# Optimization experiments

Measured on AMD Instinct MI355X. Metric: run time of the kernel, lower is better.

The kernel has to match this reference:

```python
import jax, jax.numpy as jnp
import numpy as np

B, T, C = 8, 2048, 1024   # batch, seq_len, n_embd
H = 128                   # head_size

def setup_inputs() -> dict:
    key = jax.random.key(0)
    kx, kk, kq, kv = jax.random.split(key, 4)
    scale = 1.0 / np.sqrt(C)
    return {
        "x": jax.random.normal(kx, (B, T, C), dtype=jnp.float32),
        "Wk": jax.random.normal(kk, (C, H), dtype=jnp.float32) * scale,
        "Wq": jax.random.normal(kq, (C, H), dtype=jnp.float32) * scale,
        "Wv": jax.random.normal(kv, (C, H), dtype=jnp.float32) * scale,
    }

def reference(x, Wk, Wq, Wv):
    # k,q,v: [B,T,H]
    k = x @ Wk
    q = x @ Wq
    v = x @ Wv
    # NOTE: original scales by C**-0.5 (n_embd), not head_size**-0.5
    wei = jnp.einsum("bth,bsh->bts", q, k) * (x.shape[-1] ** -0.5)  # [B,T,T]
    wei = jax.nn.softmax(wei, axis=-1)  # no causal mask in the source module
    # dropout = 0.0 -> identity
    out = jnp.einsum("bts,bsh->bth", wei, v)  # [B,T,H]
    return out
```

## Files before the change

kernel.cpp:

```cpp
#include <hip/hip_runtime.h>
#include <hip/hip_bf16.h>
#include <stdint.h>
#include <stddef.h>

#define NB 8
#define NT 2048
#define NC 1024
#define NH 128

typedef float f32x4 __attribute__((ext_vector_type(4)));
typedef short bf16x8 __attribute__((ext_vector_type(8)));
typedef short bf16x4 __attribute__((ext_vector_type(4)));

__device__ __forceinline__ unsigned short f2bf(float f) {
    union { float f; uint32_t u; } v; v.f = f;
    uint32_t u = v.u;
    u += 0x7fffu + ((u >> 16) & 1u);
    return (unsigned short)(u >> 16);
}

__device__ __forceinline__ void gld16(const void* gp, void* lp) {
    __builtin_amdgcn_global_load_lds(
        (const __attribute__((address_space(1))) unsigned int*)gp,
        (__attribute__((address_space(3))) unsigned int*)lp, 16, 0, 0);
}

__device__ __forceinline__ f32x4 mfma16(bf16x4 a, bf16x4 b, f32x4 c) {
#if __has_builtin(__builtin_amdgcn_mfma_f32_16x16x16_bf16)
    return __builtin_amdgcn_mfma_f32_16x16x16_bf16(a, b, c, 0, 0, 0);
#elif __has_builtin(__builtin_amdgcn_mfma_f32_16x16x16bf16_1k)
    return __builtin_amdgcn_mfma_f32_16x16x16bf16_1k(a, b, c, 0, 0, 0);
#else
    f32x4 d;
    asm volatile("v_mfma_f32_16x16x16_bf16 %0, %1, %2, %3"
                 : "=v"(d) : "v"(a), "v"(b), "v"(c));
    return d;
#endif
}


__global__ __launch_bounds__(256) void cast_w_kernel(const float* __restrict__ Wq,
                                                     const float* __restrict__ Wk,
                                                     const float* __restrict__ Wv,
                                                     unsigned short* __restrict__ Wtf) {
    int gid  = blockIdx.x * 256 + threadIdx.x;
    int lane = gid & 63;
    int fs   = gid >> 6;
    int kb   = fs & 31;
    int g    = fs >> 5;
    int w    = g >> 3;
    int g16  = g & 7;
    int quad = lane >> 4;
    int l16  = lane & 15;
    const float* src = (w == 0) ? Wq : ((w == 1) ? Wk : Wv);
    int n = g16 * 16 + l16;
    bf16x8 o;
#pragma unroll
    for (int j = 0; j < 8; ++j)
        o[j] = (short)f2bf(src[(size_t)(kb * 32 + quad * 8 + j) * 128 + n]);
    *(bf16x8*)(Wtf + (size_t)gid * 8) = o;
}

#define CS2 392

__global__ __launch_bounds__(512, 2) void proj_kernel(const float* __restrict__ x,
                                                      const unsigned short* __restrict__ Wtf,
                                                      unsigned short* __restrict__ Qf,
                                                      unsigned short* __restrict__ Kf,
                                                      unsigned short* __restrict__ Vf) {
    __shared__ __align__(16) unsigned short wbuf[4][24 * 512];
    __shared__ __align__(16) unsigned short abuf[2][64 * 128];

    const int tid  = threadIdx.x;
    const int wave = tid >> 6;
    const int lane = tid & 63;
    const int quad = lane >> 4;
    const int l16  = lane & 15;
    const int bidx = blockIdx.x;
    const int rowbase = bidx * 64;
    const int b    = bidx >> 5;
    const int mh   = wave & 1;
    const int nq   = wave >> 1;

    const int arow = wave * 8 + (lane >> 3);
    const float* axp = x + (size_t)(rowbase + arow) * NC;
    const int aswz = (arow & 7) << 3;
    const int rswz = (l16 & 7) << 3;

    float4 aS[2][4];
    f32x4 acc0[6] = {};
    f32x4 acc1[6] = {};

#define STAGE(KB, BI) { _Pragma("unroll") \
    for (int i_ = 0; i_ < 3; ++i_) { \
        const int g_ = wave * 3 + i_; \
        gld16(Wtf + ((size_t)(g_ * 32 + (KB)) * 512) + lane * 8, &wbuf[BI][g_ * 512]); } }

#define LOADA(C, S) { _Pragma("unroll") \
    for (int i_ = 0; i_ < 4; ++i_) \
        aS[S][i_] = *(const float4*)(axp + (C) * 128 + i_ * 32 + (lane & 7) * 4); }

#define DSWRITE(C, S) { _Pragma("unroll") \
    for (int i_ = 0; i_ < 4; ++i_) { \
        bf16x4 t_; \
        t_[0] = (short)f2bf(aS[S][i_].x); t_[1] = (short)f2bf(aS[S][i_].y); \
        t_[2] = (short)f2bf(aS[S][i_].z); t_[3] = (short)f2bf(aS[S][i_].w); \
        *(bf16x4*)(&abuf[(C) & 1][arow * 128 + ((i_ * 32 + (lane & 7) * 4) ^ aswz)]) = t_; } }

#define BARW(N) { asm volatile("s_waitcnt vmcnt(" #N ") lgkmcnt(0)" ::: "memory"); \
                  __builtin_amdgcn_s_barrier(); }

#define TICK(K, CUR) { \
    const unsigned short* ab_ = abuf[((K) >> 2) & 1]; \
    const int t2_ = ((K) & 3) * 32 + quad * 8; \
    bf16x8 af0 = *(const bf16x8*)(ab_ + (mh * 32 + l16) * 128 + (t2_ ^ rswz)); \
    bf16x8 af1 = *(const bf16x8*)(ab_ + (mh * 32 + 16 + l16) * 128 + (t2_ ^ rswz)); \
    _Pragma("unroll") \
    for (int i_ = 0; i_ < 6; ++i_) { \
        bf16x8 wf_ = *(const bf16x8*)(&wbuf[CUR][(nq * 6 + i_) * 512 + lane * 8]); \
        acc0[i_] = __builtin_amdgcn_mfma_f32_16x16x32_bf16(af0, wf_, acc0[i_], 0, 0, 0); \
        acc1[i_] = __builtin_amdgcn_mfma_f32_16x16x32_bf16(af1, wf_, acc1[i_], 0, 0, 0); } }

    LOADA(0, 0); LOADA(1, 1);
    STAGE(0, 0); STAGE(1, 1); STAGE(2, 2);
    asm volatile("s_waitcnt vmcnt(13)" ::: "memory");
    DSWRITE(0, 0);
    BARW(6);

    for (int c = 0; c < 6; ++c) {
        const int k0 = c * 4;
        LOADA(c + 2, c & 1);
        STAGE(k0 + 3, 3); TICK(k0 + 0, 0); BARW(10);
        STAGE(k0 + 4, 0); TICK(k0 + 1, 1); BARW(10);
        STAGE(k0 + 5, 1); TICK(k0 + 2, 2); BARW(6);
        STAGE(k0 + 6, 2); TICK(k0 + 3, 3); DSWRITE(c + 1, (c + 1) & 1); BARW(6);
    }
    STAGE(27, 3); TICK(24, 0); BARW(6);
    STAGE(28, 0); TICK(25, 1); BARW(6);
    STAGE(29, 1); TICK(26, 2); BARW(6);
    STAGE(30, 2); TICK(27, 3); DSWRITE(7, 1); BARW(6);
    STAGE(31, 3); TICK(28, 0); BARW(6);
    TICK(29, 1); BARW(3);
    TICK(30, 2); BARW(0);
    TICK(31, 3);
    asm volatile("s_waitcnt vmcnt(0) lgkmcnt(0)" ::: "memory");
    __builtin_amdgcn_s_barrier();

    unsigned short* cs = (unsigned short*)wbuf;
#pragma unroll
    for (int i = 0; i < 6; ++i) {
#pragma unroll
        for (int r = 0; r < 4; ++r) {
            cs[(mh * 32 +  0 + quad * 4 + r) * CS2 + nq * 96 + i * 16 + l16] = f2bf(acc0[i][r]);
            cs[(mh * 32 + 16 + quad * 4 + r) * CS2 + nq * 96 + i * 16 + l16] = f2bf(acc1[i][r]);
        }
    }
    __syncthreads();

    const int ibase = (rowbase & (NT - 1)) >> 4;
    unsigned short* qdst = Qf + (size_t)b * (NT * NH);
    unsigned short* kdst = Kf + (size_t)b * (NT * NH);
    unsigned short* vdst = Vf + (size_t)b * (NT * NH);

#pragma unroll
    for (int j = 0; j < 6; ++j) {
        const int s = wave * 6 + j;
        if (s < 32) {
            const int isK = s >> 4;
            const int t   = s & 15;
            const int m   = t >> 2;
            const int ks  = t & 3;
            unsigned short* dst = isK ? kdst : qdst;
            bf16x8 v = *(const bf16x8*)(&cs[(m * 16 + l16) * CS2 + isK * 128 + ks * 32 + quad * 8]);
            *(bf16x8*)(dst + ((size_t)((ibase + m) * 4 + ks) * 64 + lane) * 8) = v;
        } else {
            const int vv = s - 32;
            const int nt = vv >> 1;
            const int pp = vv & 1;
#pragma unroll
            for (int ff = 0; ff < 2; ++ff) {
                const int t4 = pp * 2 + ff;
                bf16x4 v;
#pragma unroll
                for (int jj = 0; jj < 4; ++jj)
                    v[jj] = (short)cs[(t4 * 16 + quad * 4 + jj) * CS2 + 256 + nt * 16 + l16];
                *(bf16x4*)(vdst + (size_t)(nt * 128 + ibase + t4) * 256 + lane * 4) = v;
            }
        }
    }

#undef TICK
#undef BARW
#undef DSWRITE
#undef LOADA
#undef STAGE
}

#define AKBUF(BI) (smem + (size_t)(BI) * 16384)
#define AVBUF(BI) (smem + (size_t)(BI) * 16384 + 8192)

__global__ __launch_bounds__(512, 1) void attn_kernel(const unsigned short* __restrict__ Qf,
                                                      const unsigned short* __restrict__ Kf,
                                                      const unsigned short* __restrict__ Vf,
                                                      float* __restrict__ out) {
    __shared__ __align__(16) unsigned short smem[3 * 16384];
    __shared__ float sl[8][32];

    const int tid  = threadIdx.x;
    const int wave = tid >> 6;
    const int lane = tid & 63;
    const int quad = lane >> 4;
    const int l16  = lane & 15;
    const int bid  = blockIdx.x;
    const int b    = bid & 7;
    const int iqg  = bid >> 3;
    const int mh   = wave & 1;
    const int kq   = wave >> 1;

    const unsigned short* qfp = Qf + (size_t)b * (NT * NH);
    const unsigned short* kfp = Kf + (size_t)b * (NT * NH);
    const unsigned short* vfp = Vf + (size_t)b * (NT * NH);

    const int iq0 = iqg * 4 + mh * 2;
    bf16x8 qf0[4], qf1[4];
#pragma unroll
    for (int ks = 0; ks < 4; ++ks) {
        qf0[ks] = *(const bf16x8*)(qfp + ((size_t)((iq0 + 0) * 4 + ks) * 64 + lane) * 8);
        qf1[ks] = *(const bf16x8*)(qfp + ((size_t)((iq0 + 1) * 4 + ks) * 64 + lane) * 8);
    }

    auto stage = [&](int j, int bi) {
#pragma unroll
        for (int i = 0; i < 4; ++i) {
            if (wave < 4) {
                const int fid = wave * 4 + i;
                gld16(kfp + ((size_t)(j * 16 + fid) * 512) + lane * 8, AKBUF(bi) + fid * 512);
            } else {
                const int sid = (wave - 4) * 4 + i;
                const int nt = sid >> 1;
                const int pp = sid & 1;
                gld16(vfp + ((size_t)(nt * 128 + j * 4 + pp * 2) * 256) + lane * 8,
                      AVBUF(bi) + (nt * 4 + pp * 2) * 256);
            }
        }
    };

    stage(0, 0);
    stage(1, 1);
    asm volatile("s_waitcnt vmcnt(4)" ::: "memory");
    __builtin_amdgcn_s_barrier();

    f32x4 O0[8] = {}, O1[8] = {};
    float ls0 = 0.f, ls1 = 0.f;
    const float scl2 = 0.03125f * 1.44269504088896340736f;

    int cur = 0;
    for (int j = 0; j < 32; ++j) {
        const int stb = (cur >= 1) ? cur - 1 : 2;
        if (j < 30) stage(j + 2, stb);
        const unsigned short* kb = AKBUF(cur);
        const unsigned short* vb = AVBUF(cur);

        f32x4 S0 = {}, S1 = {};
#pragma unroll
        for (int ks = 0; ks < 4; ++ks) {
            bf16x8 kf = *(const bf16x8*)(kb + (kq * 4 + ks) * 512 + lane * 8);
            S0 = __builtin_amdgcn_mfma_f32_16x16x32_bf16(kf, qf0[ks], S0, 0, 0, 0);
            S1 = __builtin_amdgcn_mfma_f32_16x16x32_bf16(kf, qf1[ks], S1, 0, 0, 0);
        }

        bf16x4 pf0, pf1;
#pragma unroll
        for (int r = 0; r < 4; ++r) {
            float p0 = __builtin_amdgcn_exp2f(S0[r] * scl2);
            float p1 = __builtin_amdgcn_exp2f(S1[r] * scl2);
            ls0 += p0;
            ls1 += p1;
            pf0[r] = (short)f2bf(p0);
            pf1[r] = (short)f2bf(p1);
        }

#pragma unroll
        for (int nt = 0; nt < 8; ++nt) {
            bf16x4 vf = *(const bf16x4*)(vb + (nt * 4 + kq) * 256 + lane * 4);
            O0[nt] = mfma16(pf0, vf, O0[nt]);
            O1[nt] = mfma16(pf1, vf, O1[nt]);
        }

        if (j < 30) {
            asm volatile("s_waitcnt vmcnt(4) lgkmcnt(0)" ::: "memory");
        } else {
            asm volatile("s_waitcnt vmcnt(0) lgkmcnt(0)" ::: "memory");
        }
        __builtin_amdgcn_s_barrier();
        cur = (cur >= 2) ? 0 : cur + 1;
    }

    ls0 += __shfl_xor(ls0, 16, 64);
    ls0 += __shfl_xor(ls0, 32, 64);
    ls1 += __shfl_xor(ls1, 16, 64);
    ls1 += __shfl_xor(ls1, 32, 64);
    if (quad == 0) {
        sl[wave][l16]      = ls0;
        sl[wave][16 + l16] = ls1;
    }

    float* od = (float*)smem;
    if (kq >= 2) {
        float* myod = od + (size_t)((kq - 2) * 2 + mh) * 32 * 132;
#pragma unroll
        for (int nt = 0; nt < 8; ++nt) {
#pragma unroll
            for (int r = 0; r < 4; ++r) {
                myod[(quad * 4 + r) * 132 + nt * 16 + l16]      = O0[nt][r];
                myod[(16 + quad * 4 + r) * 132 + nt * 16 + l16] = O1[nt][r];
            }
        }
    }
    __syncthreads();
    if (kq < 2) {
        const float* pod = od + (size_t)(kq * 2 + mh) * 32 * 132;
#pragma unroll
        for (int nt = 0; nt < 8; ++nt) {
#pragma unroll
            for (int r = 0; r < 4; ++r) {
                O0[nt][r] += pod[(quad * 4 + r) * 132 + nt * 16 + l16];
                O1[nt][r] += pod[(16 + quad * 4 + r) * 132 + nt * 16 + l16];
            }
        }
    }
    __syncthreads();
    if (kq == 1) {
        float* myod = od + (size_t)mh * 32 * 132;
#pragma unroll
        for (int nt = 0; nt < 8; ++nt) {
#pragma unroll
            for (int r = 0; r < 4; ++r) {
                myod[(quad * 4 + r) * 132 + nt * 16 + l16]      = O0[nt][r];
                myod[(16 + quad * 4 + r) * 132 + nt * 16 + l16] = O1[nt][r];
            }
        }
    }
    __syncthreads();

    if (kq == 0) {
        float inv0[4], inv1[4];
#pragma unroll
        for (int r = 0; r < 4; ++r) {
            const int rr = quad * 4 + r;
            inv0[r] = 1.0f / (sl[mh][rr] + sl[2 + mh][rr] +
                              sl[4 + mh][rr] + sl[6 + mh][rr]);
            inv1[r] = 1.0f / (sl[mh][16 + rr] + sl[2 + mh][16 + rr] +
                              sl[4 + mh][16 + rr] + sl[6 + mh][16 + rr]);
        }
        const float* pod = od + (size_t)mh * 32 * 132;
        float* orow = out + ((size_t)b * NT + iqg * 64 + mh * 32) * NH;
#pragma unroll
        for (int nt = 0; nt < 8; ++nt) {
#pragma unroll
            for (int r = 0; r < 4; ++r) {
                float v0 = O0[nt][r] + pod[(quad * 4 + r) * 132 + nt * 16 + l16];
                float v1 = O1[nt][r] + pod[(16 + quad * 4 + r) * 132 + nt * 16 + l16];
                orow[(quad * 4 + r) * NH + nt * 16 + l16]      = v0 * inv0[r];
                orow[(16 + quad * 4 + r) * NH + nt * 16 + l16] = v1 * inv1[r];
            }
        }
    }
}

#undef AKBUF
#undef AVBUF

extern "C" void kernel_launch(void* const* d_in, const int* in_sizes, int n_in,
                              void* d_out, int out_size, void* d_ws, size_t ws_size,
                              hipStream_t stream) {
    const float* x  = (const float*)d_in[0];
    const float* Wk = (const float*)d_in[1];
    const float* Wq = (const float*)d_in[2];
    const float* Wv = (const float*)d_in[3];
    float* out = (float*)d_out;

    char* ws = (char*)d_ws;
    unsigned short* Qf  = (unsigned short*)(ws);
    unsigned short* Kf  = (unsigned short*)(ws + 4194304);
    unsigned short* Vf  = (unsigned short*)(ws + 8388608);
    unsigned short* Wtf = (unsigned short*)(ws + 12582912);

    cast_w_kernel<<<192, 256, 0, stream>>>(Wq, Wk, Wv, Wtf);
    proj_kernel<<<256, 512, 0, stream>>>(x, Wtf, Qf, Kf, Vf);
    attn_kernel<<<256, 512, 0, stream>>>(Qf, Kf, Vf, out);
}
```

Measured before the change: 149.7 us.

## Restructure projection kernel to 32-row tiles with register-resident weight fragments

The projection kernel now uses 512 blocks of 256 threads, each computing 32 rows, instead of 256 blocks of 512 threads computing 64 rows. Weight fragments are loaded straight from global memory into registers, double-buffered two k-steps ahead, rather than staged through LDS with async global-to-LDS loads and many barriers. This cuts LDS use and barrier count and doubles the block count for better CU coverage. In exchange, each wave reads its weight slice from global/L2 with no cross-wave sharing, and global weight traffic doubles because each block covers fewer rows.

```diff
diff --git a/kernel.cpp b/kernel.cpp
--- a/kernel.cpp
+++ b/kernel.cpp
@@ -63,13 +63,12 @@
 
 #define CS2 392
 
-__global__ __launch_bounds__(512, 2) void proj_kernel(const float* __restrict__ x,
-                                                      const unsigned short* __restrict__ Wtf,
-                                                      unsigned short* __restrict__ Qf,
-                                                      unsigned short* __restrict__ Kf,
-                                                      unsigned short* __restrict__ Vf) {
-    __shared__ __align__(16) unsigned short wbuf[4][24 * 512];
-    __shared__ __align__(16) unsigned short abuf[2][64 * 128];
+__global__ __launch_bounds__(256) void proj_kernel(const float* __restrict__ x,
+                                                   const unsigned short* __restrict__ Wtf,
+                                                   unsigned short* __restrict__ Qf,
+                                                   unsigned short* __restrict__ Kf,
+                                                   unsigned short* __restrict__ Vf) {
+    __shared__ __align__(16) unsigned short smem[12800];
 
     const int tid  = threadIdx.x;
     const int wave = tid >> 6;
@@ -77,82 +76,73 @@
     const int quad = lane >> 4;
     const int l16  = lane & 15;
     const int bidx = blockIdx.x;
-    const int rowbase = bidx * 64;
-    const int b    = bidx >> 5;
-    const int mh   = wave & 1;
-    const int nq   = wave >> 1;
-
-    const int arow = wave * 8 + (lane >> 3);
+    const int rowbase = bidx * 32;
+    const int b    = bidx >> 6;
+
+    const int arow = tid >> 3;
     const float* axp = x + (size_t)(rowbase + arow) * NC;
     const int aswz = (arow & 7) << 3;
     const int rswz = (l16 & 7) << 3;
 
     float4 aS[2][4];
+    bf16x8 wA[6], wB[6];
     f32x4 acc0[6] = {};
     f32x4 acc1[6] = {};
 
-#define STAGE(KB, BI) { _Pragma("unroll") \
-    for (int i_ = 0; i_ < 3; ++i_) { \
-        const int g_ = wave * 3 + i_; \
-        gld16(Wtf + ((size_t)(g_ * 32 + (KB)) * 512) + lane * 8, &wbuf[BI][g_ * 512]); } }
+#define WLOAD(DST, KB) { _Pragma("unroll") \
+    for (int i_ = 0; i_ < 6; ++i_) \
+        DST[i_] = *(const bf16x8*)(Wtf + ((size_t)((wave * 6 + i_) * 32 + (KB)) * 512) + lane * 8); }
 
 #define LOADA(C, S) { _Pragma("unroll") \
     for (int i_ = 0; i_ < 4; ++i_) \
-        aS[S][i_] = *(const float4*)(axp + (C) * 128 + i_ * 32 + (lane & 7) * 4); }
+        aS[S][i_] = *(const float4*)(axp + (C) * 128 + i_ * 32 + (tid & 7) * 4); }
 
 #define DSWRITE(C, S) { _Pragma("unroll") \
     for (int i_ = 0; i_ < 4; ++i_) { \
         bf16x4 t_; \
         t_[0] = (short)f2bf(aS[S][i_].x); t_[1] = (short)f2bf(aS[S][i_].y); \
         t_[2] = (short)f2bf(aS[S][i_].z); t_[3] = (short)f2bf(aS[S][i_].w); \
-        *(bf16x4*)(&abuf[(C) & 1][arow * 128 + ((i_ * 32 + (lane & 7) * 4) ^ aswz)]) = t_; } }
-
-#define BARW(N) { asm volatile("s_waitcnt vmcnt(" #N ") lgkmcnt(0)" ::: "memory"); \
-                  __builtin_amdgcn_s_barrier(); }
-
-#define TICK(K, CUR) { \
-    const unsigned short* ab_ = abuf[((K) >> 2) & 1]; \
+        *(bf16x4*)(&smem[((C) & 1) * 4096 + arow * 128 + ((i_ * 32 + (tid & 7) * 4) ^ aswz)]) = t_; } }
+
+#define TICK(K, W) { \
+    const unsigned short* ab_ = smem + (((K) >> 2) & 1) * 4096; \
     const int t2_ = ((K) & 3) * 32 + quad * 8; \
-    bf16x8 af0 = *(const bf16x8*)(ab_ + (mh * 32 + l16) * 128 + (t2_ ^ rswz)); \
-    bf16x8 af1 = *(const bf16x8*)(ab_ + (mh * 32 + 16 + l16) * 128 + (t2_ ^ rswz)); \
+    bf16x8 af0 = *(const bf16x8*)(ab_ + l16 * 128 + (t2_ ^ rswz)); \
+    bf16x8 af1 = *(const bf16x8*)(ab_ + (16 + l16) * 128 + (t2_ ^ rswz)); \
     _Pragma("unroll") \
     for (int i_ = 0; i_ < 6; ++i_) { \
-        bf16x8 wf_ = *(const bf16x8*)(&wbuf[CUR][(nq * 6 + i_) * 512 + lane * 8]); \
-        acc0[i_] = __builtin_amdgcn_mfma_f32_16x16x32_bf16(af0, wf_, acc0[i_], 0, 0, 0); \
-        acc1[i_] = __builtin_amdgcn_mfma_f32_16x16x32_bf16(af1, wf_, acc1[i_], 0, 0, 0); } }
-
-    LOADA(0, 0); LOADA(1, 1);
-    STAGE(0, 0); STAGE(1, 1); STAGE(2, 2);
-    asm volatile("s_waitcnt vmcnt(13)" ::: "memory");
+        acc0[i_] = __builtin_amdgcn_mfma_f32_16x16x32_bf16(af0, W[i_], acc0[i_], 0, 0, 0); \
+        acc1[i_] = __builtin_amdgcn_mfma_f32_16x16x32_bf16(af1, W[i_], acc1[i_], 0, 0, 0); } \
+    if ((K) + 2 <= 31) WLOAD(W, (K) + 2); }
+
+#define CHUNK(C) { \
+    TICK(4*(C) + 0, wA); TICK(4*(C) + 1, wB); \
+    TICK(4*(C) + 2, wA); TICK(4*(C) + 3, wB); \
+    if ((C) < 7) { \
+        DSWRITE((C) + 1, ((C) + 1) & 1); \
+        if ((C) < 6) LOADA((C) + 2, (C) & 1); \
+        asm volatile("s_waitcnt lgkmcnt(0)" ::: "memory"); \
+        __builtin_amdgcn_s_barrier(); } }
+
+    LOADA(0, 0);
+    WLOAD(wA, 0); WLOAD(wB, 1);
     DSWRITE(0, 0);
-    BARW(6);
-
-    for (int c = 0; c < 6; ++c) {
-        const int k0 = c * 4;
-        LOADA(c + 2, c & 1);
-        STAGE(k0 + 3, 3); TICK(k0 + 0, 0); BARW(10);
-        STAGE(k0 + 4, 0); TICK(k0 + 1, 1); BARW(10);
-        STAGE(k0 + 5, 1); TICK(k0 + 2, 2); BARW(6);
-        STAGE(k0 + 6, 2); TICK(k0 + 3, 3); DSWRITE(c + 1, (c + 1) & 1); BARW(6);
-    }
-    STAGE(27, 3); TICK(24, 0); BARW(6);
-    STAGE(28, 0); TICK(25, 1); BARW(6);
-    STAGE(29, 1); TICK(26, 2); BARW(6);
-    STAGE(30, 2); TICK(27, 3); DSWRITE(7, 1); BARW(6);
-    STAGE(31, 3); TICK(28, 0); BARW(6);
-    TICK(29, 1); BARW(3);
-    TICK(30, 2); BARW(0);
-    TICK(31, 3);
-    asm volatile("s_waitcnt vmcnt(0) lgkmcnt(0)" ::: "memory");
+    LOADA(1, 1);
+    asm volatile("s_waitcnt lgkmcnt(0)" ::: "memory");
     __builtin_amdgcn_s_barrier();
 
-    unsigned short* cs = (unsigned short*)wbuf;
+    CHUNK(0); CHUNK(1); CHUNK(2); CHUNK(3);
+    CHUNK(4); CHUNK(5); CHUNK(6); CHUNK(7);
+
+    __syncthreads();
+
+    unsigned short* cs = smem;
 #pragma unroll
     for (int i = 0; i < 6; ++i) {
 #pragma unroll
         for (int r = 0; r < 4; ++r) {
-            cs[(mh * 32 +  0 + quad * 4 + r) * CS2 + nq * 96 + i * 16 + l16] = f2bf(acc0[i][r]);
-            cs[(mh * 32 + 16 + quad * 4 + r) * CS2 + nq * 96 + i * 16 + l16] = f2bf(acc1[i][r]);
+            cs[(quad * 4 + r) * CS2 + wave * 96 + i * 16 + l16]      = f2bf(acc0[i][r]);
+            cs[(16 + quad * 4 + r) * CS2 + wave * 96 + i * 16 + l16] = f2bf(acc1[i][r]);
         }
     }
     __syncthreads();
@@ -162,38 +152,36 @@
     unsigned short* kdst = Kf + (size_t)b * (NT * NH);
     unsigned short* vdst = Vf + (size_t)b * (NT * NH);
 
-#pragma unroll
-    for (int j = 0; j < 6; ++j) {
-        const int s = wave * 6 + j;
-        if (s < 32) {
-            const int isK = s >> 4;
-            const int t   = s & 15;
-            const int m   = t >> 2;
-            const int ks  = t & 3;
-            unsigned short* dst = isK ? kdst : qdst;
-            bf16x8 v = *(const bf16x8*)(&cs[(m * 16 + l16) * CS2 + isK * 128 + ks * 32 + quad * 8]);
-            *(bf16x8*)(dst + ((size_t)((ibase + m) * 4 + ks) * 64 + lane) * 8) = v;
-        } else {
-            const int vv = s - 32;
-            const int nt = vv >> 1;
-            const int pp = vv & 1;
-#pragma unroll
-            for (int ff = 0; ff < 2; ++ff) {
-                const int t4 = pp * 2 + ff;
-                bf16x4 v;
-#pragma unroll
-                for (int jj = 0; jj < 4; ++jj)
-                    v[jj] = (short)cs[(t4 * 16 + quad * 4 + jj) * CS2 + 256 + nt * 16 + l16];
-                *(bf16x4*)(vdst + (size_t)(nt * 128 + ibase + t4) * 256 + lane * 4) = v;
-            }
-        }
-    }
-
+    {
+        const int mq   = wave & 1;
+        const int isK  = wave >> 1;
+        unsigned short* dst = isK ? kdst : qdst;
+        const int off = isK * 128;
+        const int iqt = ibase + mq;
+#pragma unroll
+        for (int ks = 0; ks < 4; ++ks) {
+            bf16x8 v = *(const bf16x8*)(&cs[(mq * 16 + l16) * CS2 + off + ks * 32 + quad * 8]);
+            *(bf16x8*)(dst + ((size_t)(iqt * 4 + ks) * 64 + lane) * 8) = v;
+        }
+    }
+#pragma unroll
+    for (int i = 0; i < 2; ++i) {
+        const int nt = wave * 2 + i;
+#pragma unroll
+        for (int tkl = 0; tkl < 2; ++tkl) {
+            bf16x4 v;
+#pragma unroll
+            for (int jj = 0; jj < 4; ++jj)
+                v[jj] = (short)cs[(tkl * 16 + quad * 4 + jj) * CS2 + 256 + nt * 16 + l16];
+            *(bf16x4*)(vdst + (size_t)(nt * 128 + ibase + tkl) * 256 + lane * 4) = v;
+        }
+    }
+
+#undef CHUNK
 #undef TICK
-#undef BARW
 #undef DSWRITE
 #undef LOADA
-#undef STAGE
+#undef WLOAD
 }
 
 #define AKBUF(BI) (smem + (size_t)(BI) * 16384)
@@ -387,6 +375,6 @@
     unsigned short* Wtf = (unsigned short*)(ws + 12582912);
 
     cast_w_kernel<<<192, 256, 0, stream>>>(Wq, Wk, Wv, Wtf);
-    proj_kernel<<<256, 512, 0, stream>>>(x, Wtf, Qf, Kf, Vf);
+    proj_kernel<<<512, 256, 0, stream>>>(x, Wtf, Qf, Kf, Vf);
     attn_kernel<<<256, 512, 0, stream>>>(Qf, Kf, Vf, out);
 }
```

Measured after the change: 157.5 us. 1.05x slower.
